# Optimization experiments

Measured on AMD Instinct MI355X. Metric: run time of the kernel, lower is better.

Reference implementation:

```python
import jax, jax.numpy as jnp
import numpy as np

GRAD_CLIP = 50.0
MIN_DIST = 1e-10


def _logpsi(x_flat, W1, b1, W2, b2, w3):
    # x_flat: [D] flattened electron coordinates -> scalar log|psi|
    h = jnp.tanh(x_flat @ W1 + b1)
    h = jnp.tanh(h @ W2 + b2)
    return h @ w3


def setup_inputs() -> dict:
    key = jax.random.key(0)
    k = jax.random.split(key, 6)
    B, NE, H = 1024, 16, 512
    D = NE * 3
    electron_coords = jax.random.normal(k[0], (B, NE, 3), dtype=jnp.float32)
    atom_coords = jnp.asarray(
        [[0.0, 0.0, 0.0], [1.4, 0.0, 0.0], [0.0, 1.4, 0.0], [0.0, 0.0, 1.4]],
        dtype=jnp.float32)
    nuclear_charges = jnp.ones((4,), dtype=jnp.float32)
    W1 = jax.random.normal(k[1], (D, H), dtype=jnp.float32) / np.float32(np.sqrt(D))
    b1 = jnp.zeros((H,), dtype=jnp.float32)
    W2 = jax.random.normal(k[2], (H, H), dtype=jnp.float32) / np.float32(np.sqrt(H))
    b2 = jnp.zeros((H,), dtype=jnp.float32)
    w3 = jax.random.normal(k[3], (H,), dtype=jnp.float32) / np.float32(np.sqrt(H))
    return {"electron_coords": electron_coords, "atom_coords": atom_coords,
            "nuclear_charges": nuclear_charges,
            "W1": W1, "b1": b1, "W2": W2, "b2": b2, "w3": w3}


def _kinetic_log(electron_coords, W1, b1, W2, b2, w3):
    # kinetic = -0.5 * (lap log psi + |grad log psi|^2), per batch element
    B, NE, _ = electron_coords.shape
    D = NE * 3
    x = electron_coords.reshape(B, D)

    def f(xi):
        return _logpsi(xi, W1, b1, W2, b2, w3)

    def per_sample(xi):
        g = jax.grad(f)(xi)                       # [D]
        hdiag = jnp.diagonal(jax.jacfwd(jax.grad(f))(xi))  # [D]
        return g, hdiag

    g, hdiag = jax.vmap(per_sample)(x)            # [B, D] each
    hdiag = jnp.where(jnp.isfinite(hdiag),
                      jnp.clip(hdiag, -GRAD_CLIP, GRAD_CLIP), 0.0)
    lap = hdiag.sum(-1)
    gsq = (g ** 2).sum(-1)
    return jnp.clip(-0.5 * (lap + gsq), -100.0, 100.0)


def _potential(electron_coords, atom_coords, nuclear_charges):
    B, NE, _ = electron_coords.shape
    NA = atom_coords.shape[0]
    # electron-electron repulsion, sum over i<j
    d_ee = electron_coords[:, :, None, :] - electron_coords[:, None, :, :]
    r_ee = jnp.sqrt((d_ee ** 2).sum(-1) + jnp.eye(NE, dtype=electron_coords.dtype))
    r_ee = jnp.maximum(r_ee, MIN_DIST)
    iu = jnp.triu(jnp.ones((NE, NE), dtype=bool), 1)
    e_e = jnp.where(iu, 1.0 / r_ee, 0.0).sum((1, 2))
    # electron-nucleus attraction
    d_en = electron_coords[:, :, None, :] - atom_coords[None, None, :, :]
    r_en = jnp.maximum(jnp.sqrt((d_en ** 2).sum(-1)), MIN_DIST)  # [B, NE, NA]
    e_n = -(nuclear_charges[None, None, :] / r_en).sum((1, 2))
    # nucleus-nucleus repulsion (constant over batch)
    d_nn = atom_coords[:, None, :] - atom_coords[None, :, :]
    r_nn = jnp.sqrt((d_nn ** 2).sum(-1) + jnp.eye(NA, dtype=atom_coords.dtype))
    iun = jnp.triu(jnp.ones((NA, NA), dtype=bool), 1)
    zz = nuclear_charges[:, None] * nuclear_charges[None, :]
    n_n = jnp.where(iun & (r_nn > MIN_DIST), zz / r_nn, 0.0).sum()
    return jnp.clip(e_e + e_n + n_n, -1000.0, 1000.0)


def reference(electron_coords, atom_coords, nuclear_charges, W1, b1, W2, b2, w3):
    kinetic = _kinetic_log(electron_coords, W1, b1, W2, b2, w3)
    potential = _potential(electron_coords, atom_coords, nuclear_charges)
    return kinetic + potential
```

## Files before the change

### kernel.cpp

```cpp
#include <hip/hip_runtime.h>
#include <math.h>

#define BTOT 1024
#define NE   16
#define NA   4
#define DD   48
#define HH   512
#define ROWS (BTOT * DD)

#define GBM2 256
#define GBN  128
#define GBK  64
#define NCB  (HH / GBN)
#define MG2  (NCB * (ROWS / GBM2))
#define NU   128
#define NT   (HH / GBK)

typedef __attribute__((ext_vector_type(8))) short bf16x8;
typedef __attribute__((ext_vector_type(8))) unsigned short u16x8;
typedef __attribute__((ext_vector_type(4))) float f32x4;

__device__ inline unsigned short f2bf(float f) {
  unsigned int u = __builtin_bit_cast(unsigned int, f);
  u += 0x7fffu + ((u >> 16) & 1u);
  return (unsigned short)(u >> 16);
}
__device__ inline float bf2f(unsigned short s) {
  unsigned int u = ((unsigned int)s) << 16;
  return __builtin_bit_cast(float, u);
}

__device__ inline int swz(int row, int chunk) {
  return (row << 6) + ((chunk ^ (row & 7)) << 3);
}

__device__ inline void gload16(const ushort* g, ushort* l) {
  __builtin_amdgcn_global_load_lds(
      (const __attribute__((address_space(1))) unsigned int*)g,
      (__attribute__((address_space(3))) unsigned int*)l, 16, 0, 0);
}

__device__ inline void gemm64_k_loop(const ushort* __restrict__ abase,
                                     const ushort* __restrict__ bbase,
                                     ushort* As, ushort* Bs,
                                     int w, int l, f32x4 acc[2][2]) {
  const int lrow = l >> 3;
  const int cg = (l & 7) ^ lrow;
  const ushort* __restrict__ ap = abase + (w * 16 + lrow) * HH + cg * 8;
  const ushort* __restrict__ bp = bbase + (w * 16 + lrow) * HH + cg * 8;
  const int wm = w >> 1, wn = w & 1;
  const int lr = l & 15, lg = l >> 4;

#pragma unroll
  for (int q = 0; q < 2; ++q) {
    gload16(ap + q * 8 * HH, As + (w * 2 + q) * 512);
    gload16(bp + q * 8 * HH, Bs + (w * 2 + q) * 512);
  }
  __syncthreads();

  for (int kt = 0; kt < NT; ++kt) {
    const int cur = (kt & 1) << 12;
    if (kt + 1 < NT) {
      const int nxt = ((kt + 1) & 1) << 12;
      const int koff = (kt + 1) * GBK;
#pragma unroll
      for (int q = 0; q < 2; ++q) {
        gload16(ap + koff + q * 8 * HH, As + nxt + (w * 2 + q) * 512);
        gload16(bp + koff + q * 8 * HH, Bs + nxt + (w * 2 + q) * 512);
      }
    }
#pragma unroll
    for (int k0 = 0; k0 < GBK; k0 += 32) {
      const int ck = (k0 >> 3) + lg;
      bf16x8 af[2], bfr[2];
#pragma unroll
      for (int m = 0; m < 2; ++m)
        af[m] = *reinterpret_cast<const bf16x8*>(
            &As[cur + swz(wm * 32 + m * 16 + lr, ck)]);
#pragma unroll
      for (int n = 0; n < 2; ++n)
        bfr[n] = *reinterpret_cast<const bf16x8*>(
            &Bs[cur + swz(wn * 32 + n * 16 + lr, ck)]);
#pragma unroll
      for (int m = 0; m < 2; ++m)
#pragma unroll
        for (int n = 0; n < 2; ++n)
          acc[m][n] = __builtin_amdgcn_mfma_f32_16x16x32_bf16(af[m], bfr[n],
                                                              acc[m][n], 0, 0, 0);
    }
    __syncthreads();
  }
}

__global__ __launch_bounds__(256) void k_l1pot(
    const float* __restrict__ X, const float* __restrict__ ATOM,
    const float* __restrict__ Z, const float* __restrict__ W1,
    const float* __restrict__ B1, const float* __restrict__ W2,
    ushort* __restrict__ W2b, ushort* __restrict__ W2Tb,
    ushort* __restrict__ T1b, float* __restrict__ D1,
    ushort* __restrict__ Ab, float* __restrict__ POT) {
  const int b = blockIdx.x, tid = threadIdx.x;
  __shared__ float xs[DD];
  __shared__ float d1s[HH];
  __shared__ float red[256];
  __shared__ float tile[32][33];

  if (b < 256) {
    const int bx = (b & 15) * 32, by = (b >> 4) * 32;
    const int tx = tid & 31, ty = tid >> 5;
    for (int r = 0; r < 32; r += 8) {
      float v = W2[(by + ty + r) * HH + bx + tx];
      tile[ty + r][tx] = v;
      W2b[(by + ty + r) * HH + bx + tx] = f2bf(v);
    }
    __syncthreads();
    for (int r = 0; r < 32; r += 8)
      W2Tb[(bx + ty + r) * HH + by + tx] = f2bf(tile[tx][ty + r]);
  }

  if (tid < DD) xs[tid] = X[b * DD + tid];
  __syncthreads();

  {
    const int j0 = tid * 2;
    float acc0 = B1[j0], acc1 = B1[j0 + 1];
#pragma unroll 8
    for (int i = 0; i < DD; ++i) {
      float xv = xs[i];
      float2 w = *reinterpret_cast<const float2*>(&W1[i * HH + j0]);
      acc0 = fmaf(xv, w.x, acc0);
      acc1 = fmaf(xv, w.y, acc1);
    }
    float t0 = tanhf(acc0), t1v = tanhf(acc1);
    unsigned int pk = ((unsigned int)f2bf(t1v) << 16) | f2bf(t0);
    *reinterpret_cast<unsigned int*>(&T1b[b * HH + j0]) = pk;
    float dd0 = 1.f - t0 * t0, dd1 = 1.f - t1v * t1v;
    d1s[j0] = dd0; d1s[j0 + 1] = dd1;
    *reinterpret_cast<float2*>(&D1[b * HH + j0]) = make_float2(dd0, dd1);
  }
  __syncthreads();

  {
    const int k0 = tid * 2;
    const float dd0 = d1s[k0], dd1 = d1s[k0 + 1];
#pragma unroll 4
    for (int i = 0; i < DD; ++i) {
      float2 w = *reinterpret_cast<const float2*>(&W1[i * HH + k0]);
      unsigned int pk =
          ((unsigned int)f2bf(w.y * dd1) << 16) | f2bf(w.x * dd0);
      *reinterpret_cast<unsigned int*>(&Ab[(b * DD + i) * HH + k0]) = pk;
    }
  }

  {
    float p = 0.f;
    for (int pr = tid; pr < NE * (NE - 1) / 2; pr += 256) {
      int i = 0, rem = pr;
      while (rem >= NE - 1 - i) { rem -= NE - 1 - i; ++i; }
      int j = i + 1 + rem;
      float dx = xs[i * 3 + 0] - xs[j * 3 + 0];
      float dy = xs[i * 3 + 1] - xs[j * 3 + 1];
      float dz = xs[i * 3 + 2] - xs[j * 3 + 2];
      float r = fmaxf(sqrtf(dx * dx + dy * dy + dz * dz), 1e-10f);
      p += 1.f / r;
    }
    for (int idx = tid; idx < NE * NA; idx += 256) {
      int e = idx / NA, a = idx % NA;
      float dx = xs[e * 3 + 0] - ATOM[a * 3 + 0];
      float dy = xs[e * 3 + 1] - ATOM[a * 3 + 1];
      float dz = xs[e * 3 + 2] - ATOM[a * 3 + 2];
      float r = fmaxf(sqrtf(dx * dx + dy * dy + dz * dz), 1e-10f);
      p -= Z[a] / r;
    }
    if (tid == 0) {
      for (int a = 0; a < NA; ++a)
        for (int a2 = a + 1; a2 < NA; ++a2) {
          float dx = ATOM[a * 3 + 0] - ATOM[a2 * 3 + 0];
          float dy = ATOM[a * 3 + 1] - ATOM[a2 * 3 + 1];
          float dz = ATOM[a * 3 + 2] - ATOM[a2 * 3 + 2];
          float r = sqrtf(dx * dx + dy * dy + dz * dz);
          if (r > 1e-10f) p += Z[a] * Z[a2] / r;
        }
    }
    red[tid] = p;
    __syncthreads();
    for (int s = 128; s > 0; s >>= 1) {
      if (tid < s) red[tid] += red[tid + s];
      __syncthreads();
    }
    if (tid == 0) POT[b] = fminf(fmaxf(red[0], -1000.f), 1000.f);
  }
}

__global__ __launch_bounds__(256) void k_act64(
    const ushort* __restrict__ Ab, const ushort* __restrict__ Bb,
    const float* __restrict__ B2, const float* __restrict__ w3,
    float* __restrict__ C2, ushort* __restrict__ Vb) {
  const int rb = blockIdx.x >> 3;
  const int cb = blockIdx.x & 7;
  const int row0 = rb * 64, col0 = cb * 64;
  const int t = threadIdx.x, w = t >> 6, l = t & 63;

  __shared__ ushort As[2 * 64 * GBK];
  __shared__ ushort Bs[2 * 64 * GBK];

  f32x4 acc[2][2];
#pragma unroll
  for (int m = 0; m < 2; ++m)
#pragma unroll
    for (int n = 0; n < 2; ++n) acc[m][n] = (f32x4)0.f;

  gemm64_k_loop(Ab + row0 * HH, Bb + col0 * HH, As, Bs, w, l, acc);

  const int wm = w >> 1, wn = w & 1, lr = l & 15, lg = l >> 4;
#pragma unroll
  for (int m = 0; m < 2; ++m)
#pragma unroll
    for (int e = 0; e < 4; ++e) {
      const int row = row0 + wm * 32 + m * 16 + lg * 4 + e;
#pragma unroll
      for (int n = 0; n < 2; ++n) {
        const int col = col0 + wn * 32 + n * 16 + lr;
        float a2 = acc[m][n][e] + B2[col];
        float t2 = tanhf(a2);
        float d2 = 1.f - t2 * t2;
        float w3v = w3[col];
        C2[row * HH + col] = -2.f * t2 * d2 * w3v;
        Vb[row * HH + col] = f2bf(w3v * d2);
      }
    }
}

__global__ __launch_bounds__(512) void k_mu(
    const ushort* __restrict__ Abig, const ushort* __restrict__ W2Tb,
    const float* __restrict__ C2, float* __restrict__ HD2P,
    const ushort* __restrict__ Vb, const ushort* __restrict__ W2b,
    const float* __restrict__ D1, const ushort* __restrict__ T1b,
    float* __restrict__ S1, ushort* __restrict__ C1b) {
  const int t = threadIdx.x, w = t >> 6, l = t & 63;
  __shared__ ushort As[2 * GBM2 * GBK];
  __shared__ ushort Bs[2 * GBN * GBK];

  const int lrow = l >> 3;
  const int cg = (l & 7) ^ lrow;
  const int lr = l & 15, lg = l >> 4;

  if (blockIdx.x < NU) {
    const int ub = blockIdx.x;
    const int rb = ub >> 3, cb = ub & 7;
    const int row0 = rb * 64, col0 = cb * 64;
    const ushort* __restrict__ ap = Vb  + (row0 + w * 8 + lrow) * HH + cg * 8;
    const ushort* __restrict__ bp = W2b + (col0 + w * 8 + lrow) * HH + cg * 8;
    const int wm = w >> 2, wn = w & 3;

    f32x4 acc[2];
    acc[0] = (f32x4)0.f; acc[1] = (f32x4)0.f;

    gload16(ap, As + w * 512);
    gload16(bp, Bs + w * 512);
    __syncthreads();

    for (int kt = 0; kt < NT; ++kt) {
      const int curA = (kt & 1) << 14, curB = (kt & 1) << 13;
      if (kt + 1 < NT) {
        const int nA = ((kt + 1) & 1) << 14, nB = ((kt + 1) & 1) << 13;
        const int koff = (kt + 1) * GBK;
        gload16(ap + koff, As + nA + w * 512);
        gload16(bp + koff, Bs + nB + w * 512);
      }
#pragma unroll
      for (int k0 = 0; k0 < GBK; k0 += 32) {
        const int ck = (k0 >> 3) + lg;
        bf16x8 af0 = *reinterpret_cast<const bf16x8*>(
            &As[curA + swz(wm * 32 + lr, ck)]);
        bf16x8 af1 = *reinterpret_cast<const bf16x8*>(
            &As[curA + swz(wm * 32 + 16 + lr, ck)]);
        bf16x8 bf = *reinterpret_cast<const bf16x8*>(
            &Bs[curB + swz(wn * 16 + lr, ck)]);
        acc[0] = __builtin_amdgcn_mfma_f32_16x16x32_bf16(af0, bf, acc[0], 0, 0, 0);
        acc[1] = __builtin_amdgcn_mfma_f32_16x16x32_bf16(af1, bf, acc[1], 0, 0, 0);
      }
      __syncthreads();
    }

#pragma unroll
    for (int m = 0; m < 2; ++m)
#pragma unroll
      for (int e = 0; e < 4; ++e) {
        const int row = row0 + wm * 32 + m * 16 + lg * 4 + e;
        const int col = col0 + wn * 16 + lr;
        float u = acc[m][e];
        float d1 = D1[row * HH + col];
        float t1 = bf2f(T1b[row * HH + col]);
        S1[row * HH + col] = d1 * u;
        C1b[row * HH + col] = f2bf(-2.f * t1 * d1 * u);
      }
  } else {
    const int bid = blockIdx.x - NU;
    const int wgid = (bid & 7) * (MG2 / 8) + (bid >> 3);
    const int cb = wgid & 3;
    const int rb = wgid >> 2;
    const int row0 = rb * GBM2, col0 = cb * GBN;
    const ushort* __restrict__ ap = Abig + (row0 + w * 32 + lrow) * HH + cg * 8;
    const ushort* __restrict__ bp = W2Tb + (col0 + w * 16 + lrow) * HH + cg * 8;
    const int wm = w >> 1, wn = w & 1;

    f32x4 acc[4][4];
#pragma unroll
    for (int m = 0; m < 4; ++m)
#pragma unroll
      for (int n = 0; n < 4; ++n) acc[m][n] = (f32x4)0.f;

#pragma unroll
    for (int q = 0; q < 4; ++q)
      gload16(ap + q * 8 * HH, As + (w * 4 + q) * 512);
#pragma unroll
    for (int q = 0; q < 2; ++q)
      gload16(bp + q * 8 * HH, Bs + (w * 2 + q) * 512);
    __syncthreads();

    for (int kt = 0; kt < NT; ++kt) {
      const int curA = (kt & 1) << 14, curB = (kt & 1) << 13;
      if (kt + 1 < NT) {
        const int nA = ((kt + 1) & 1) << 14, nB = ((kt + 1) & 1) << 13;
        const int koff = (kt + 1) * GBK;
#pragma unroll
        for (int q = 0; q < 4; ++q)
          gload16(ap + koff + q * 8 * HH, As + nA + (w * 4 + q) * 512);
#pragma unroll
        for (int q = 0; q < 2; ++q)
          gload16(bp + koff + q * 8 * HH, Bs + nB + (w * 2 + q) * 512);
      }
#pragma unroll
      for (int k0 = 0; k0 < GBK; k0 += 32) {
        const int ck = (k0 >> 3) + lg;
        bf16x8 af[4], bfr[4];
#pragma unroll
        for (int m = 0; m < 4; ++m)
          af[m] = *reinterpret_cast<const bf16x8*>(
              &As[curA + swz(wm * 64 + m * 16 + lr, ck)]);
#pragma unroll
        for (int n = 0; n < 4; ++n)
          bfr[n] = *reinterpret_cast<const bf16x8*>(
              &Bs[curB + swz(wn * 64 + n * 16 + lr, ck)]);
#pragma unroll
        for (int m = 0; m < 4; ++m)
#pragma unroll
          for (int n = 0; n < 4; ++n)
            acc[m][n] = __builtin_amdgcn_mfma_f32_16x16x32_bf16(af[m], bfr[n],
                                                                acc[m][n], 0, 0, 0);
      }
      __syncthreads();
    }

#pragma unroll
    for (int m = 0; m < 4; ++m) {
#pragma unroll
      for (int e = 0; e < 4; ++e) {
        const int row_g = row0 + wm * 64 + m * 16 + lg * 4 + e;
        const int bs2 = row_g / DD;
        const float* __restrict__ c2p = &C2[bs2 * HH + col0 + wn * 64 + lr];
        float s = 0.f;
#pragma unroll
        for (int n = 0; n < 4; ++n) {
          float mv = acc[m][n][e];
          s = fmaf(c2p[n * 16] * mv, mv, s);
        }
        s += __shfl_xor(s, 1);
        s += __shfl_xor(s, 2);
        s += __shfl_xor(s, 4);
        s += __shfl_xor(s, 8);
        if (lr == 0) HD2P[cb * ROWS + row_g] = s;
      }
    }
  }
}

__global__ __launch_bounds__(256) void k_grad_fin(
    const float* __restrict__ W1, const float* __restrict__ S1,
    const ushort* __restrict__ C1b, const float* __restrict__ HD2P,
    const float* __restrict__ POT, float* __restrict__ OUT) {
  const int b = blockIdx.x, tid = threadIdx.x;
  __shared__ float gtmp[DD], htmp[DD];
  const int wid = tid >> 6, lane = tid & 63;
  const int j0 = lane * 8;

  for (int i = wid; i < DD; i += 4) {
    float4 wa = *reinterpret_cast<const float4*>(&W1[i * HH + j0]);
    float4 wb = *reinterpret_cast<const float4*>(&W1[i * HH + j0 + 4]);
    float4 sa = *reinterpret_cast<const float4*>(&S1[b * HH + j0]);
    float4 sb = *reinterpret_cast<const float4*>(&S1[b * HH + j0 + 4]);
    u16x8 cv = *reinterpret_cast<const u16x8*>(&C1b[b * HH + j0]);
    float wv[8] = {wa.x, wa.y, wa.z, wa.w, wb.x, wb.y, wb.z, wb.w};
    float sv[8] = {sa.x, sa.y, sa.z, sa.w, sb.x, sb.y, sb.z, sb.w};
    float gp = 0.f, hp = 0.f;
#pragma unroll
    for (int e = 0; e < 8; ++e) {
      gp = fmaf(wv[e], sv[e], gp);
      hp = fmaf(wv[e] * wv[e], bf2f(cv[e]), hp);
    }
#pragma unroll
    for (int off = 32; off > 0; off >>= 1) {
      gp += __shfl_down(gp, off);
      hp += __shfl_down(hp, off);
    }
    if (lane == 0) { gtmp[i] = gp; htmp[i] = hp; }
  }
  __syncthreads();

  if (tid < 64) {
    float gv = 0.f, hv = 0.f;
    if (tid < DD) {
      gv = gtmp[tid];
      float h = htmp[tid];
#pragma unroll
      for (int c = 0; c < NCB; ++c) h += HD2P[c * ROWS + b * DD + tid];
      if (h >= -1e30f && h <= 1e30f) h = fminf(fmaxf(h, -50.f), 50.f);
      else h = 0.f;
      hv = h;
    }
    float sq = gv * gv;
#pragma unroll
    for (int off = 32; off > 0; off >>= 1) {
      sq += __shfl_down(sq, off);
      hv += __shfl_down(hv, off);
    }
    if (tid == 0) {
      float kin = fminf(fmaxf(-0.5f * (hv + sq), -100.f), 100.f);
      OUT[b] = kin + POT[b];
    }
  }
}

extern "C" void kernel_launch(void* const* d_in, const int* in_sizes, int n_in,
                              void* d_out, int out_size, void* d_ws, size_t ws_size,
                              hipStream_t stream) {
  const float* X    = (const float*)d_in[0];
  const float* ATOM = (const float*)d_in[1];
  const float* Z    = (const float*)d_in[2];
  const float* W1   = (const float*)d_in[3];
  const float* B1   = (const float*)d_in[4];
  const float* W2   = (const float*)d_in[5];
  const float* B2   = (const float*)d_in[6];
  const float* w3   = (const float*)d_in[7];
  float* out = (float*)d_out;

  float* ws = (float*)d_ws;
  ushort* W2b  = (ushort*)(ws + 0);
  ushort* W2Tb = (ushort*)(ws + 131072);
  ushort* T1b  = (ushort*)(ws + 262144);
  ushort* Vb   = (ushort*)(ws + 524288);
  ushort* C1b  = (ushort*)(ws + 786432);
  float*  S1   = ws + 1048576;
  float*  D1   = ws + 1572864;
  float*  C2   = ws + 2097152;
  float*  POT  = ws + 2621440;
  float*  HD2P = ws + 2622464;
  ushort* Abig = (ushort*)(ws + 2819072);

  k_l1pot<<<BTOT, 256, 0, stream>>>(X, ATOM, Z, W1, B1, W2, W2b, W2Tb,
                                    T1b, D1, Abig, POT);
  k_act64<<<128, 256, 0, stream>>>(T1b, W2Tb, B2, w3, C2, Vb);
  k_mu<<<NU + MG2, 512, 0, stream>>>(Abig, W2Tb, C2, HD2P,
                                     Vb, W2b, D1, T1b, S1, C1b);
  k_grad_fin<<<BTOT, 256, 0, stream>>>(W1, S1, C1b, HD2P, POT, out);
}
```

Before: 99.31 us.

## Deepen GEMM prefetch to two tiles ahead and vectorize Ab construction

The GEMM main loop now issues the global-to-LDS loads for tile kt+2 after the compute barrier. Partial vmcnt waits let one tile stay in flight while the current one is consumed, and s_setprio raises priority during the MFMA section. This is meant to hide more global load latency behind MFMA work, at the cost of two barriers per iteration. Separately, the Ab construction in the prologue kernel now has each thread produce 8 bf16 values with 16-byte loads and stores, cutting the number of memory instructions.

```diff
diff --git a/kernel.cpp b/kernel.cpp
--- a/kernel.cpp
+++ b/kernel.cpp
@@ -141,14 +141,19 @@
   __syncthreads();
 
   {
-    const int k0 = tid * 2;
-    const float dd0 = d1s[k0], dd1 = d1s[k0 + 1];
-#pragma unroll 4
-    for (int i = 0; i < DD; ++i) {
-      float2 w = *reinterpret_cast<const float2*>(&W1[i * HH + k0]);
-      unsigned int pk =
-          ((unsigned int)f2bf(w.y * dd1) << 16) | f2bf(w.x * dd0);
-      *reinterpret_cast<unsigned int*>(&Ab[(b * DD + i) * HH + k0]) = pk;
+    const int k0 = (tid & 63) * 8;
+    float d[8];
+#pragma unroll
+    for (int e = 0; e < 8; ++e) d[e] = d1s[k0 + e];
+    for (int i = (tid >> 6); i < DD; i += 4) {
+      float4 wa = *reinterpret_cast<const float4*>(&W1[i * HH + k0]);
+      float4 wb = *reinterpret_cast<const float4*>(&W1[i * HH + k0 + 4]);
+      u16x8 pk;
+      pk[0] = f2bf(wa.x * d[0]); pk[1] = f2bf(wa.y * d[1]);
+      pk[2] = f2bf(wa.z * d[2]); pk[3] = f2bf(wa.w * d[3]);
+      pk[4] = f2bf(wb.x * d[4]); pk[5] = f2bf(wb.y * d[5]);
+      pk[6] = f2bf(wb.z * d[6]); pk[7] = f2bf(wb.w * d[7]);
+      *reinterpret_cast<u16x8*>(&Ab[(b * DD + i) * HH + k0]) = pk;
     }
   }
 
@@ -317,20 +322,20 @@
 #pragma unroll
     for (int q = 0; q < 2; ++q)
       gload16(bp + q * 8 * HH, Bs + (w * 2 + q) * 512);
-    __syncthreads();
+#pragma unroll
+    for (int q = 0; q < 4; ++q)
+      gload16(ap + GBK + q * 8 * HH, As + 16384 + (w * 4 + q) * 512);
+#pragma unroll
+    for (int q = 0; q < 2; ++q)
+      gload16(bp + GBK + q * 8 * HH, Bs + 8192 + (w * 2 + q) * 512);
+    asm volatile("s_waitcnt vmcnt(6)" ::: "memory");
+    __builtin_amdgcn_sched_barrier(0);
+    __builtin_amdgcn_s_barrier();
+    __builtin_amdgcn_sched_barrier(0);
 
     for (int kt = 0; kt < NT; ++kt) {
       const int curA = (kt & 1) << 14, curB = (kt & 1) << 13;
-      if (kt + 1 < NT) {
-        const int nA = ((kt + 1) & 1) << 14, nB = ((kt + 1) & 1) << 13;
-        const int koff = (kt + 1) * GBK;
-#pragma unroll
-        for (int q = 0; q < 4; ++q)
-          gload16(ap + koff + q * 8 * HH, As + nA + (w * 4 + q) * 512);
-#pragma unroll
-        for (int q = 0; q < 2; ++q)
-          gload16(bp + koff + q * 8 * HH, Bs + nB + (w * 2 + q) * 512);
-      }
+      __builtin_amdgcn_s_setprio(1);
 #pragma unroll
       for (int k0 = 0; k0 < GBK; k0 += 32) {
         const int ck = (k0 >> 3) + lg;
@@ -350,7 +355,25 @@
             acc[m][n] = __builtin_amdgcn_mfma_f32_16x16x32_bf16(af[m], bfr[n],
                                                                 acc[m][n], 0, 0, 0);
       }
-      __syncthreads();
+      __builtin_amdgcn_s_setprio(0);
+      __builtin_amdgcn_sched_barrier(0);
+      __builtin_amdgcn_s_barrier();
+      __builtin_amdgcn_sched_barrier(0);
+      if (kt + 2 < NT) {
+        const int koff = (kt + 2) * GBK;
+#pragma unroll
+        for (int q = 0; q < 4; ++q)
+          gload16(ap + koff + q * 8 * HH, As + curA + (w * 4 + q) * 512);
+#pragma unroll
+        for (int q = 0; q < 2; ++q)
+          gload16(bp + koff + q * 8 * HH, Bs + curB + (w * 2 + q) * 512);
+        asm volatile("s_waitcnt vmcnt(6)" ::: "memory");
+      } else {
+        asm volatile("s_waitcnt vmcnt(0)" ::: "memory");
+      }
+      __builtin_amdgcn_sched_barrier(0);
+      __builtin_amdgcn_s_barrier();
+      __builtin_amdgcn_sched_barrier(0);
     }
 
 #pragma unroll
```

Measured after the change: 100.2 us. Within noise of the previous version (+0.9%).

## Build W1·D1 operand on the fly in GEMM instead of materializing Abig

Applied to the files above, without the earlier changes.

The layer-1 kernel no longer writes the large bf16 Abig tensor, which had one row per (sample, input dim) pair. The big GEMM path in k_mu now builds each A tile itself: it loads W1 and D1 in fp32, multiplies them, converts to bf16 and stores the result in LDS. This removes a large global write and a later read of that intermediate. In exchange, the A and B tiles lose their double buffering, so global loads no longer overlap with MFMA work and each k-step adds extra VALU conversion.

```diff
diff --git a/kernel.cpp b/kernel.cpp
--- a/kernel.cpp
+++ b/kernel.cpp
@@ -98,10 +98,9 @@
     const float* __restrict__ B1, const float* __restrict__ W2,
     ushort* __restrict__ W2b, ushort* __restrict__ W2Tb,
     ushort* __restrict__ T1b, float* __restrict__ D1,
-    ushort* __restrict__ Ab, float* __restrict__ POT) {
+    float* __restrict__ POT) {
   const int b = blockIdx.x, tid = threadIdx.x;
   __shared__ float xs[DD];
-  __shared__ float d1s[HH];
   __shared__ float red[256];
   __shared__ float tile[32][33];
 
@@ -134,22 +133,8 @@
     float t0 = tanhf(acc0), t1v = tanhf(acc1);
     unsigned int pk = ((unsigned int)f2bf(t1v) << 16) | f2bf(t0);
     *reinterpret_cast<unsigned int*>(&T1b[b * HH + j0]) = pk;
-    float dd0 = 1.f - t0 * t0, dd1 = 1.f - t1v * t1v;
-    d1s[j0] = dd0; d1s[j0 + 1] = dd1;
-    *reinterpret_cast<float2*>(&D1[b * HH + j0]) = make_float2(dd0, dd1);
-  }
-  __syncthreads();
-
-  {
-    const int k0 = tid * 2;
-    const float dd0 = d1s[k0], dd1 = d1s[k0 + 1];
-#pragma unroll 4
-    for (int i = 0; i < DD; ++i) {
-      float2 w = *reinterpret_cast<const float2*>(&W1[i * HH + k0]);
-      unsigned int pk =
-          ((unsigned int)f2bf(w.y * dd1) << 16) | f2bf(w.x * dd0);
-      *reinterpret_cast<unsigned int*>(&Ab[(b * DD + i) * HH + k0]) = pk;
-    }
+    *reinterpret_cast<float2*>(&D1[b * HH + j0]) =
+        make_float2(1.f - t0 * t0, 1.f - t1v * t1v);
   }
 
   {
@@ -232,14 +217,15 @@
 }
 
 __global__ __launch_bounds__(512) void k_mu(
-    const ushort* __restrict__ Abig, const ushort* __restrict__ W2Tb,
-    const float* __restrict__ C2, float* __restrict__ HD2P,
+    const float* __restrict__ W1, const ushort* __restrict__ W2Tb,
+    const float* __restrict__ D1, const float* __restrict__ C2,
+    float* __restrict__ HD2P,
     const ushort* __restrict__ Vb, const ushort* __restrict__ W2b,
-    const float* __restrict__ D1, const ushort* __restrict__ T1b,
+    const ushort* __restrict__ T1b,
     float* __restrict__ S1, ushort* __restrict__ C1b) {
   const int t = threadIdx.x, w = t >> 6, l = t & 63;
-  __shared__ ushort As[2 * GBM2 * GBK];
-  __shared__ ushort Bs[2 * GBN * GBK];
+  __shared__ ushort As[GBM2 * GBK];
+  __shared__ ushort Bs[GBN * GBK];
 
   const int lrow = l >> 3;
   const int cg = (l & 7) ^ lrow;
@@ -261,9 +247,9 @@
     __syncthreads();
 
     for (int kt = 0; kt < NT; ++kt) {
-      const int curA = (kt & 1) << 14, curB = (kt & 1) << 13;
+      const int curA = (kt & 1) << 12, curB = (kt & 1) << 12;
       if (kt + 1 < NT) {
-        const int nA = ((kt + 1) & 1) << 14, nB = ((kt + 1) & 1) << 13;
+        const int nA = ((kt + 1) & 1) << 12, nB = ((kt + 1) & 1) << 12;
         const int koff = (kt + 1) * GBK;
         gload16(ap + koff, As + nA + w * 512);
         gload16(bp + koff, Bs + nB + w * 512);
@@ -301,36 +287,47 @@
     const int cb = wgid & 3;
     const int rb = wgid >> 2;
     const int row0 = rb * GBM2, col0 = cb * GBN;
-    const ushort* __restrict__ ap = Abig + (row0 + w * 32 + lrow) * HH + cg * 8;
     const ushort* __restrict__ bp = W2Tb + (col0 + w * 16 + lrow) * HH + cg * 8;
     const int wm = w >> 1, wn = w & 1;
 
+    const float* w1p[4];
+    const float* d1p[4];
+    int aaddr[4];
+#pragma unroll
+    for (int q = 0; q < 4; ++q) {
+      const int idx = t + 512 * q;
+      const int r = idx >> 3, c = idx & 7;
+      const int gr = row0 + r;
+      const int s = gr / DD, rw = gr - s * DD;
+      w1p[q] = W1 + rw * HH + c * 8;
+      d1p[q] = D1 + s * HH + c * 8;
+      aaddr[q] = swz(r, c);
+    }
+
     f32x4 acc[4][4];
 #pragma unroll
     for (int m = 0; m < 4; ++m)
 #pragma unroll
       for (int n = 0; n < 4; ++n) acc[m][n] = (f32x4)0.f;
 
-#pragma unroll
-    for (int q = 0; q < 4; ++q)
-      gload16(ap + q * 8 * HH, As + (w * 4 + q) * 512);
-#pragma unroll
-    for (int q = 0; q < 2; ++q)
-      gload16(bp + q * 8 * HH, Bs + (w * 2 + q) * 512);
-    __syncthreads();
-
-    for (int kt = 0; kt < NT; ++kt) {
-      const int curA = (kt & 1) << 14, curB = (kt & 1) << 13;
-      if (kt + 1 < NT) {
-        const int nA = ((kt + 1) & 1) << 14, nB = ((kt + 1) & 1) << 13;
-        const int koff = (kt + 1) * GBK;
-#pragma unroll
-        for (int q = 0; q < 4; ++q)
-          gload16(ap + koff + q * 8 * HH, As + nA + (w * 4 + q) * 512);
-#pragma unroll
-        for (int q = 0; q < 2; ++q)
-          gload16(bp + koff + q * 8 * HH, Bs + nB + (w * 2 + q) * 512);
-      }
+    for (int kt = 0; kt < HH; kt += GBK) {
+#pragma unroll
+      for (int q = 0; q < 2; ++q)
+        gload16(bp + kt + q * 8 * HH, Bs + (w * 2 + q) * 512);
+#pragma unroll
+      for (int q = 0; q < 4; ++q) {
+        float4 wa = *reinterpret_cast<const float4*>(w1p[q] + kt);
+        float4 wb = *reinterpret_cast<const float4*>(w1p[q] + kt + 4);
+        float4 da = *reinterpret_cast<const float4*>(d1p[q] + kt);
+        float4 db = *reinterpret_cast<const float4*>(d1p[q] + kt + 4);
+        u16x8 pk;
+        pk[0] = f2bf(wa.x * da.x); pk[1] = f2bf(wa.y * da.y);
+        pk[2] = f2bf(wa.z * da.z); pk[3] = f2bf(wa.w * da.w);
+        pk[4] = f2bf(wb.x * db.x); pk[5] = f2bf(wb.y * db.y);
+        pk[6] = f2bf(wb.z * db.z); pk[7] = f2bf(wb.w * db.w);
+        *reinterpret_cast<u16x8*>(&As[aaddr[q]]) = pk;
+      }
+      __syncthreads();
 #pragma unroll
       for (int k0 = 0; k0 < GBK; k0 += 32) {
         const int ck = (k0 >> 3) + lg;
@@ -338,11 +335,11 @@
 #pragma unroll
         for (int m = 0; m < 4; ++m)
           af[m] = *reinterpret_cast<const bf16x8*>(
-              &As[curA + swz(wm * 64 + m * 16 + lr, ck)]);
+              &As[swz(wm * 64 + m * 16 + lr, ck)]);
 #pragma unroll
         for (int n = 0; n < 4; ++n)
           bfr[n] = *reinterpret_cast<const bf16x8*>(
-              &Bs[curB + swz(wn * 64 + n * 16 + lr, ck)]);
+              &Bs[swz(wn * 64 + n * 16 + lr, ck)]);
 #pragma unroll
         for (int m = 0; m < 4; ++m)
 #pragma unroll
@@ -456,12 +453,11 @@
   float*  C2   = ws + 2097152;
   float*  POT  = ws + 2621440;
   float*  HD2P = ws + 2622464;
-  ushort* Abig = (ushort*)(ws + 2819072);
 
   k_l1pot<<<BTOT, 256, 0, stream>>>(X, ATOM, Z, W1, B1, W2, W2b, W2Tb,
-                                    T1b, D1, Abig, POT);
+                                    T1b, D1, POT);
   k_act64<<<128, 256, 0, stream>>>(T1b, W2Tb, B2, w3, C2, Vb);
-  k_mu<<<NU + MG2, 512, 0, stream>>>(Abig, W2Tb, C2, HD2P,
-                                     Vb, W2b, D1, T1b, S1, C1b);
+  k_mu<<<NU + MG2, 512, 0, stream>>>(W1, W2Tb, D1, C2, HD2P,
+                                     Vb, W2b, T1b, S1, C1b);
   k_grad_fin<<<BTOT, 256, 0, stream>>>(W1, S1, C1b, HD2P, POT, out);
 }
```

After: 119.9 us. 20.7% more time.
